# Kernel optimization log

Measured on AMD Instinct MI355X. Metric: run time of the kernel, lower is better.

## Reference

```python
import jax, jax.numpy as jnp
import numpy as np

LEAKY_SLOPE = 0.2  # tf.nn.leaky_relu default alpha


def setup_inputs() -> dict:
    key = jax.random.key(0)
    k1, k2, k3 = jax.random.split(key, 3)
    B, T, K, D = 64, 2048, 256, 256  # batch, timesteps, n_nodes, out_dim
    inputs = jax.random.normal(k1, (B, T, K), dtype=jnp.float32)
    W = jax.random.normal(k2, (K, D), dtype=jnp.float32) * (1.0 / np.sqrt(K))
    a = jax.random.normal(k3, (2 * D, 1), dtype=jnp.float32) * (1.0 / np.sqrt(2 * D))
    return {"inputs": inputs, "W": W, "a": a}


def reference(inputs, W, a):
    # inputs: (B, T, K); W: (K, D); a: (2D, 1)
    B, T, K = inputs.shape
    D = W.shape[1]
    H = jnp.matmul(inputs, W)  # (B, T, D)
    # Original: H_concat[b,t,k] = concat([H[b,t], H[b,t]]) for every k (both
    # repeats are of the same H), so H_concat @ a == H @ (a_i + a_j), constant in k.
    a_i = a[:D, 0]
    a_j = a[D:, 0]
    e = jax.nn.leaky_relu(H @ (a_i + a_j), negative_slope=LEAKY_SLOPE)  # (B, T)
    e = jnp.broadcast_to(e[:, :, None], (B, T, K))  # (B, T, K) -- constant along K
    alpha = jax.nn.softmax(e, axis=2)  # exactly uniform 1/K
    # sum_k alpha[b,t,k] * H[b,t,d]  (H_repeat_i[b,t,k,:] == H[b,t,:])
    H_gat = jnp.einsum('btk,btd->btd', alpha, H)  # (B, T, D)
    return H_gat
```

## Files before the change

kernel.cpp:

```cpp
#include <hip/hip_runtime.h>
#include <hip/hip_bf16.h>
#include <cstdint>


static constexpr int MTOT = 64 * 2048;
static constexpr int KDIM = 256;
static constexpr int NDIM = 256;

typedef __bf16 bf16x8 __attribute__((ext_vector_type(8)));
typedef float f32x4 __attribute__((ext_vector_type(4)));

__device__ __forceinline__ uint32_t f2bf_pk(float a, float b) {
    uint32_t ua = __float_as_uint(a);
    uint32_t ub = __float_as_uint(b);
    ua = ua + 0x7fffu + ((ua >> 16) & 1u);
    ub = ub + 0x7fffu + ((ub >> 16) & 1u);
    return (ua >> 16) | (ub & 0xffff0000u);
}

__global__ void wt_transpose(const float* __restrict__ W, unsigned short* __restrict__ Wt) {
    int n = blockIdx.x;
    int k = threadIdx.x;
    float v = W[k * NDIM + n];
    uint32_t u = __float_as_uint(v);
    u = u + 0x7fffu + ((u >> 16) & 1u);
    Wt[n * KDIM + k] = (unsigned short)(u >> 16);
}

__global__ __launch_bounds__(512, 4)
void gat_gemm(const float* __restrict__ A, const unsigned short* __restrict__ Wt,
              float* __restrict__ C) {
    __shared__ alignas(16) unsigned short As[128 * 72];
    __shared__ alignas(16) unsigned short Bs[256 * 72];

    const int tid  = threadIdx.x;
    const int lane = tid & 63;
    const int wave = tid >> 6;
    const int l15  = lane & 15;
    const int quad = lane >> 4;
    const int wm   = wave >> 2;
    const int wn   = wave & 3;

    const int bm = blockIdx.x * 128;

    const int arow = tid >> 2;
    const int aseg = tid & 3;
    const int brow = tid >> 3;
    const int bseg = tid & 7;

    f32x4 acc[4][4];
#pragma unroll
    for (int i = 0; i < 4; ++i)
#pragma unroll
        for (int j = 0; j < 4; ++j)
            acc[i][j] = (f32x4)0.0f;

    for (int kt = 0; kt < 4; ++kt) {
        const int k0 = kt * 64;

        const float4* ap = (const float4*)(A + (size_t)(bm + arow) * KDIM + k0 + aseg * 16);
        float4 a0 = ap[0], a1 = ap[1], a2 = ap[2], a3 = ap[3];

        const unsigned short* bp = Wt + (size_t)brow * KDIM + k0 + bseg * 8;
        uint4 b0 = *(const uint4*)(bp);
        uint4 b1 = *(const uint4*)(bp + 64 * KDIM);
        uint4 b2 = *(const uint4*)(bp + 128 * KDIM);
        uint4 b3 = *(const uint4*)(bp + 192 * KDIM);

        if (kt) __syncthreads();

        {
            uint4 w0, w1;
            w0.x = f2bf_pk(a0.x, a0.y); w0.y = f2bf_pk(a0.z, a0.w);
            w0.z = f2bf_pk(a1.x, a1.y); w0.w = f2bf_pk(a1.z, a1.w);
            w1.x = f2bf_pk(a2.x, a2.y); w1.y = f2bf_pk(a2.z, a2.w);
            w1.z = f2bf_pk(a3.x, a3.y); w1.w = f2bf_pk(a3.z, a3.w);
            uint4* dst = (uint4*)&As[arow * 72 + aseg * 16];
            dst[0] = w0;
            dst[1] = w1;
        }
        *(uint4*)&Bs[(brow +   0) * 72 + bseg * 8] = b0;
        *(uint4*)&Bs[(brow +  64) * 72 + bseg * 8] = b1;
        *(uint4*)&Bs[(brow + 128) * 72 + bseg * 8] = b2;
        *(uint4*)&Bs[(brow + 192) * 72 + bseg * 8] = b3;

        __syncthreads();

#pragma unroll
        for (int ks = 0; ks < 2; ++ks) {
            bf16x8 af[4];
#pragma unroll
            for (int i = 0; i < 4; ++i)
                af[i] = *(const bf16x8*)&As[(wm * 64 + i * 16 + l15) * 72 + ks * 32 + quad * 8];
#pragma unroll
            for (int j = 0; j < 4; ++j) {
                bf16x8 bfj = *(const bf16x8*)&Bs[(wn * 64 + j * 16 + l15) * 72 + ks * 32 + quad * 8];
#pragma unroll
                for (int i = 0; i < 4; ++i)
                    acc[i][j] = __builtin_amdgcn_mfma_f32_16x16x32_bf16(af[i], bfj, acc[i][j], 0, 0, 0);
            }
        }
    }

#pragma unroll
    for (int i = 0; i < 4; ++i) {
#pragma unroll
        for (int j = 0; j < 4; ++j) {
            const int n = wn * 64 + j * 16 + l15;
            const size_t mbase = (size_t)(bm + wm * 64 + i * 16 + quad * 4);
#pragma unroll
            for (int r = 0; r < 4; ++r)
                C[(mbase + r) * NDIM + n] = acc[i][j][r];
        }
    }
}

extern "C" void kernel_launch(void* const* d_in, const int* in_sizes, int n_in,
                              void* d_out, int out_size, void* d_ws, size_t ws_size,
                              hipStream_t stream) {
    (void)in_sizes; (void)n_in; (void)out_size; (void)ws_size;
    const float* inputs = (const float*)d_in[0];
    const float* W      = (const float*)d_in[1];
    unsigned short* Wt = (unsigned short*)d_ws;
    float* out = (float*)d_out;

    hipLaunchKernelGGL(wt_transpose, dim3(NDIM), dim3(KDIM), 0, stream, W, Wt);
    hipLaunchKernelGGL(gat_gemm, dim3(MTOT / 128), dim3(512), 0, stream, inputs, Wt, out);
}
```

Baseline: 244.1 us.

## Keep full bf16 W resident in LDS and stream A fragments directly from global

Changes the weight-prep kernel to write W as an MFMA-friendly packed image of 8-element k-groups, which each block copies whole (128 KB) into LDS once. Each wave now owns 16 rows and loads its A fragments straight from global memory into registers, converting them to bf16 in-register and prefetching the next k-slice. This removes the per-k-tile A staging through LDS and its barriers. The cost is 1024-thread blocks with one block per CU because of the LDS footprint, less reuse of B fragments per LDS read, and 16 accumulators per wave.

```diff
diff --git a/kernel.cpp b/kernel.cpp
--- a/kernel.cpp
+++ b/kernel.cpp
@@ -1,5 +1,4 @@
 #include <hip/hip_runtime.h>
-#include <hip/hip_bf16.h>
 #include <cstdint>
 
 
@@ -18,100 +17,74 @@
     return (ua >> 16) | (ub & 0xffff0000u);
 }
 
-__global__ void wt_transpose(const float* __restrict__ W, unsigned short* __restrict__ Wt) {
-    int n = blockIdx.x;
-    int k = threadIdx.x;
+__global__ void wt_image(const float* __restrict__ W, unsigned short* __restrict__ img) {
+    int k = blockIdx.x;
+    int n = threadIdx.x;
     float v = W[k * NDIM + n];
     uint32_t u = __float_as_uint(v);
     u = u + 0x7fffu + ((u >> 16) & 1u);
-    Wt[n * KDIM + k] = (unsigned short)(u >> 16);
+    img[((size_t)((k >> 3) * NDIM + n) << 3) + (k & 7)] = (unsigned short)(u >> 16);
 }
 
-__global__ __launch_bounds__(512, 4)
-void gat_gemm(const float* __restrict__ A, const unsigned short* __restrict__ Wt,
+__global__ __launch_bounds__(1024)
+void gat_gemm(const float* __restrict__ A, const uint4* __restrict__ img,
               float* __restrict__ C) {
-    __shared__ alignas(16) unsigned short As[128 * 72];
-    __shared__ alignas(16) unsigned short Bs[256 * 72];
+    __shared__ uint4 Bs[8192];
 
-    const int tid  = threadIdx.x;
+    const int tid = threadIdx.x;
+
+#pragma unroll
+    for (int i = 0; i < 8; ++i)
+        Bs[tid + i * 1024] = img[tid + i * 1024];
+
     const int lane = tid & 63;
     const int wave = tid >> 6;
     const int l15  = lane & 15;
     const int quad = lane >> 4;
-    const int wm   = wave >> 2;
-    const int wn   = wave & 3;
 
-    const int bm = blockIdx.x * 128;
+    const int row = blockIdx.x * 256 + wave * 16 + l15;
+    const float* arow = A + (size_t)row * KDIM;
 
-    const int arow = tid >> 2;
-    const int aseg = tid & 3;
-    const int brow = tid >> 3;
-    const int bseg = tid & 7;
+    f32x4 acc[16];
+#pragma unroll
+    for (int j = 0; j < 16; ++j) acc[j] = (f32x4)0.0f;
 
-    f32x4 acc[4][4];
-#pragma unroll
-    for (int i = 0; i < 4; ++i)
-#pragma unroll
-        for (int j = 0; j < 4; ++j)
-            acc[i][j] = (f32x4)0.0f;
+    __syncthreads();
 
-    for (int kt = 0; kt < 4; ++kt) {
-        const int k0 = kt * 64;
-
-        const float4* ap = (const float4*)(A + (size_t)(bm + arow) * KDIM + k0 + aseg * 16);
-        float4 a0 = ap[0], a1 = ap[1], a2 = ap[2], a3 = ap[3];
-
-        const unsigned short* bp = Wt + (size_t)brow * KDIM + k0 + bseg * 8;
-        uint4 b0 = *(const uint4*)(bp);
-        uint4 b1 = *(const uint4*)(bp + 64 * KDIM);
-        uint4 b2 = *(const uint4*)(bp + 128 * KDIM);
-        uint4 b3 = *(const uint4*)(bp + 192 * KDIM);
-
-        if (kt) __syncthreads();
-
-        {
-            uint4 w0, w1;
-            w0.x = f2bf_pk(a0.x, a0.y); w0.y = f2bf_pk(a0.z, a0.w);
-            w0.z = f2bf_pk(a1.x, a1.y); w0.w = f2bf_pk(a1.z, a1.w);
-            w1.x = f2bf_pk(a2.x, a2.y); w1.y = f2bf_pk(a2.z, a2.w);
-            w1.z = f2bf_pk(a3.x, a3.y); w1.w = f2bf_pk(a3.z, a3.w);
-            uint4* dst = (uint4*)&As[arow * 72 + aseg * 16];
-            dst[0] = w0;
-            dst[1] = w1;
-        }
-        *(uint4*)&Bs[(brow +   0) * 72 + bseg * 8] = b0;
-        *(uint4*)&Bs[(brow +  64) * 72 + bseg * 8] = b1;
-        *(uint4*)&Bs[(brow + 128) * 72 + bseg * 8] = b2;
-        *(uint4*)&Bs[(brow + 192) * 72 + bseg * 8] = b3;
-
-        __syncthreads();
+    float4 a0 = *(const float4*)(arow + quad * 8);
+    float4 a1 = *(const float4*)(arow + quad * 8 + 4);
 
 #pragma unroll
-        for (int ks = 0; ks < 2; ++ks) {
-            bf16x8 af[4];
+    for (int ks = 0; ks < 8; ++ks) {
+        float4 n0, n1;
+        if (ks < 7) {
+            const float* p = arow + (ks + 1) * 32 + quad * 8;
+            n0 = *(const float4*)(p);
+            n1 = *(const float4*)(p + 4);
+        }
+
+        uint4 ap;
+        ap.x = f2bf_pk(a0.x, a0.y); ap.y = f2bf_pk(a0.z, a0.w);
+        ap.z = f2bf_pk(a1.x, a1.y); ap.w = f2bf_pk(a1.z, a1.w);
+        bf16x8 af = __builtin_bit_cast(bf16x8, ap);
+
+        const uint4* bbase = &Bs[(ks * 4 + quad) * 256 + l15];
 #pragma unroll
-            for (int i = 0; i < 4; ++i)
-                af[i] = *(const bf16x8*)&As[(wm * 64 + i * 16 + l15) * 72 + ks * 32 + quad * 8];
-#pragma unroll
-            for (int j = 0; j < 4; ++j) {
-                bf16x8 bfj = *(const bf16x8*)&Bs[(wn * 64 + j * 16 + l15) * 72 + ks * 32 + quad * 8];
-#pragma unroll
-                for (int i = 0; i < 4; ++i)
-                    acc[i][j] = __builtin_amdgcn_mfma_f32_16x16x32_bf16(af[i], bfj, acc[i][j], 0, 0, 0);
-            }
+        for (int j = 0; j < 16; ++j) {
+            bf16x8 bf = __builtin_bit_cast(bf16x8, bbase[j * 16]);
+            acc[j] = __builtin_amdgcn_mfma_f32_16x16x32_bf16(af, bf, acc[j], 0, 0, 0);
         }
+
+        a0 = n0; a1 = n1;
     }
 
+    const size_t rbase = (size_t)(blockIdx.x * 256 + wave * 16 + quad * 4);
 #pragma unroll
-    for (int i = 0; i < 4; ++i) {
+    for (int j = 0; j < 16; ++j) {
+        const int n = j * 16 + l15;
 #pragma unroll
-        for (int j = 0; j < 4; ++j) {
-            const int n = wn * 64 + j * 16 + l15;
-            const size_t mbase = (size_t)(bm + wm * 64 + i * 16 + quad * 4);
-#pragma unroll
-            for (int r = 0; r < 4; ++r)
-                C[(mbase + r) * NDIM + n] = acc[i][j][r];
-        }
+        for (int r = 0; r < 4; ++r)
+            C[(rbase + r) * NDIM + n] = acc[j][r];
     }
 }
 
@@ -121,9 +94,10 @@
     (void)in_sizes; (void)n_in; (void)out_size; (void)ws_size;
     const float* inputs = (const float*)d_in[0];
     const float* W      = (const float*)d_in[1];
-    unsigned short* Wt = (unsigned short*)d_ws;
+    unsigned short* img = (unsigned short*)d_ws;
     float* out = (float*)d_out;
 
-    hipLaunchKernelGGL(wt_transpose, dim3(NDIM), dim3(KDIM), 0, stream, W, Wt);
-    hipLaunchKernelGGL(gat_gemm, dim3(MTOT / 128), dim3(512), 0, stream, inputs, Wt, out);
+    hipLaunchKernelGGL(wt_image, dim3(KDIM), dim3(NDIM), 0, stream, W, img);
+    hipLaunchKernelGGL(gat_gemm, dim3(MTOT / 256), dim3(1024), 0, stream,
+                       inputs, (const uint4*)img, out);
 }
```

Result: no change. 247.2 us (+1.3%).
